# Optimization experiments

Measured on AMD Instinct MI355X. Metric: run time of the kernel, lower is better.

Reference implementation:

```python
import jax, jax.numpy as jnp
import numpy as np

NUM_USERS = 100000
NUM_ITEMS = 200000
IN_DIM = 128
HID = 256
E = 500000


def setup_inputs() -> dict:
    key = jax.random.key(0)
    ks = jax.random.split(key, 12)
    s1 = 1.0 / np.sqrt(2 * IN_DIM)
    s2 = 1.0 / np.sqrt(HID)
    return {
        "user_embed": jax.random.normal(ks[0], (NUM_USERS, IN_DIM), jnp.float32),
        "item_embed": jax.random.normal(ks[1], (NUM_ITEMS, IN_DIM), jnp.float32),
        "u_clicks": jax.random.randint(ks[2], (E,), 0, NUM_USERS, jnp.int32),
        "v_clicks": jax.random.randint(ks[3], (E,), 0, NUM_ITEMS, jnp.int32),
        "u_buys": jax.random.randint(ks[4], (E,), 0, NUM_USERS, jnp.int32),
        "v_buys": jax.random.randint(ks[5], (E,), 0, NUM_ITEMS, jnp.int32),
        "W1_clicks": jax.random.normal(ks[6], (2 * IN_DIM, HID), jnp.float32) * s1,
        "b1_clicks": jnp.zeros((HID,), jnp.float32),
        "W2_clicks": jax.random.normal(ks[7], (HID,), jnp.float32) * s2,
        "b2_clicks": jnp.zeros((1,), jnp.float32),
        "W1_buys": jax.random.normal(ks[8], (2 * IN_DIM, HID), jnp.float32) * s1,
        "b1_buys": jnp.zeros((HID,), jnp.float32),
        "W2_buys": jax.random.normal(ks[9], (HID,), jnp.float32) * s2,
        "b2_buys": jnp.zeros((1,), jnp.float32),
    }


def _edge_mlp(h_u, h_v, W1, b1, W2, b2):
    # concat([h_u, h_v]) @ W1 computed without materializing the concat:
    # split W1 into source-half and target-half. Dropout(p=0) is identity.
    d = h_u.shape[1]
    h = jax.nn.relu(h_u @ W1[:d] + h_v @ W1[d:] + b1)  # [E, HID]
    return h @ W2 + b2[0]  # [E] (Linear(hidden,1).squeeze(1))


def reference(user_embed, item_embed, u_clicks, v_clicks, u_buys, v_buys,
              W1_clicks, b1_clicks, W2_clicks, b2_clicks,
              W1_buys, b1_buys, W2_buys, b2_buys):
    logits_clicks = _edge_mlp(user_embed[u_clicks], item_embed[v_clicks],
                              W1_clicks, b1_clicks, W2_clicks, b2_clicks)
    logits_buys = _edge_mlp(user_embed[u_buys], item_embed[v_buys],
                            W1_buys, b1_buys, W2_buys, b2_buys)
    return logits_clicks, logits_buys
```

## Files before the change

kernel.cpp:

```cpp
#include <hip/hip_runtime.h>
#include <hip/hip_bf16.h>

typedef short bf16x8 __attribute__((ext_vector_type(8)));
typedef float f32x4 __attribute__((ext_vector_type(4)));
typedef unsigned int u32x4 __attribute__((ext_vector_type(4)));

#define HID 256
#define IN_DIM 128
#define M_BLOCK 64
#define NPERSIST 256

__device__ __forceinline__ float bf2f(unsigned short x) {
    union { unsigned int u; float f; } c; c.u = ((unsigned int)x) << 16; return c.f;
}
__device__ __forceinline__ unsigned short f2bf(float f) {
    union { float f; unsigned int u; } c; c.f = f;
    unsigned int u = c.u;
    u += 0x7FFFu + ((u >> 16) & 1u);
    return (unsigned short)(u >> 16);
}
__device__ __forceinline__ unsigned int pack2(float lo, float hi) {
    return (unsigned int)f2bf(lo) | ((unsigned int)f2bf(hi) << 16);
}

__device__ __forceinline__ void gload_lds16(const void* g, void* l) {
    __builtin_amdgcn_global_load_lds(
        (const __attribute__((address_space(1))) void*)g,
        (__attribute__((address_space(3))) void*)l,
        16, 0, 0);
}

__device__ __forceinline__ bool detect_bf16(const unsigned short* p, int strideElems) {
    const int lane = threadIdx.x & 63;
    unsigned int u = p[(size_t)2 * lane * strideElems];
    unsigned int e = (u >> 7) & 0xFFu;
    bool bad = ((u & 0x7FFFu) != 0u) && (e < 90u || e > 141u);
    return __ballot(bad) == 0ull;
}
__device__ __forceinline__ bool detect_idx64(const int* p) {
    const int lane = threadIdx.x & 63;
    int v = p[2 * (lane * 64) + 1];
    return __ballot(v != 0) == 0ull;
}

extern "C" __global__ void cvt_tables_kernel(
    const void* __restrict__ user_embed, const void* __restrict__ item_embed,
    unsigned short* __restrict__ uT, unsigned short* __restrict__ iT,
    long long nU8, long long nI8)
{
    const int t = blockIdx.y;
    const void* src = t ? item_embed : user_embed;
    unsigned short* dst = t ? iT : uT;
    const long long n8 = t ? nI8 : nU8;
    const bool bf = detect_bf16((const unsigned short*)src, 1024);
    long long i = (long long)blockIdx.x * 256 + threadIdx.x;
    const long long stride = (long long)gridDim.x * 256;
    if (bf) {
        const u32x4* s = (const u32x4*)src;
        for (; i < n8; i += stride)
            __builtin_nontemporal_store(s[i], reinterpret_cast<u32x4*>(dst + i * 8));
    } else {
        const float4* s = (const float4*)src;
        for (; i < n8; i += stride) {
            float4 f0 = s[2 * i];
            float4 f1 = s[2 * i + 1];
            u32x4 o;
            o.x = pack2(f0.x, f0.y);
            o.y = pack2(f0.z, f0.w);
            o.z = pack2(f1.x, f1.y);
            o.w = pack2(f1.z, f1.w);
            __builtin_nontemporal_store(o, reinterpret_cast<u32x4*>(dst + i * 8));
        }
    }
}

extern "C" __global__ void pack_w1_kernel(
    const void* __restrict__ W1c,
    const void* __restrict__ W1b,
    unsigned short* __restrict__ outp)
{
    const int t = blockIdx.y;
    const void* W1 = t ? W1b : W1c;
    const unsigned short* W1u = (const unsigned short*)W1;
    const float* W1f = (const float*)W1;
    const bool w1bf = detect_bf16(W1u, 512);

    const int tid = blockIdx.x * 256 + threadIdx.x;
    const int lane = tid & 63;
    const int nt = (tid >> 6) & 15;
    const int kt = tid >> 10;
    const int k0 = kt * 32 + (lane >> 4) * 8;
    const int n  = nt * 16 + (lane & 15);
    unsigned short vals[8];
#pragma unroll
    for (int j = 0; j < 8; ++j) {
        const int src = (k0 + j) * HID + n;
        vals[j] = w1bf ? W1u[src] : f2bf(W1f[src]);
    }
    unsigned short* dst = outp + (size_t)t * 65536 + (size_t)tid * 8;
    *reinterpret_cast<uint4*>(dst) = *reinterpret_cast<const uint4*>(vals);
}

extern "C" __global__ __launch_bounds__(256, 2)
void edge_mlp_kernel(
    const void* __restrict__ user_embed,
    const void* __restrict__ item_embed,
    const unsigned short* __restrict__ uT,
    const unsigned short* __restrict__ iT,
    const int* __restrict__ u0, const int* __restrict__ v0,
    const int* __restrict__ u1, const int* __restrict__ v1,
    const unsigned short* __restrict__ packedW1,
    const void* __restrict__ b1_0, const void* __restrict__ w2_0,
    const void* __restrict__ b2_0,
    const void* __restrict__ b1_1, const void* __restrict__ w2_1,
    const void* __restrict__ b2_1,
    float* __restrict__ out, int E, int useWs)
{
    __shared__ __attribute__((aligned(16))) unsigned short sA[2][32 * 64 * 8];
    __shared__ float pRed[4][M_BLOCK];

    const int t   = blockIdx.y;
    const int tid = threadIdx.x;
    const int lane = tid & 63;
    const int wv   = tid >> 6;
    const int lq = lane >> 4;
    const int lm = lane & 15;

    const int* uI = t ? u1 : u0;
    const int* vI = t ? v1 : v0;
    const void* b1 = t ? b1_1 : b1_0;
    const void* w2 = t ? w2_1 : w2_0;
    const void* b2 = t ? b2_1 : b2_0;
    const unsigned short* pW = packedW1 + (size_t)t * 65536;

    const bool w2Bf = detect_bf16((const unsigned short*)w2, 2);

    const int* gI = (wv < 2) ? uI : vI;
    const bool g64 = detect_idx64(gI);
    const int halfOff = (wv & 1) * 64;
    const unsigned short* tabW = (wv < 2) ? uT : iT;
    const void* tabRaw = (wv < 2) ? user_embed : item_embed;
    bool tbf = false;
    if (!useWs) tbf = detect_bf16((const unsigned short*)tabRaw, 1024);

    bf16x8 bFr[8][4];
#pragma unroll
    for (int kt = 0; kt < 8; ++kt)
#pragma unroll
        for (int ntg = 0; ntg < 4; ++ntg)
            bFr[kt][ntg] = *reinterpret_cast<const bf16x8*>(
                pW + (((size_t)(kt * 16 + wv * 4 + ntg) * 64 + lane) * 8));

    float b1v[4], w2v[4];
#pragma unroll
    for (int ntg = 0; ntg < 4; ++ntg) {
        const int n = (wv * 4 + ntg) * 16 + lm;
        b1v[ntg] = w2Bf ? bf2f(((const unsigned short*)b1)[n]) : ((const float*)b1)[n];
        w2v[ntg] = w2Bf ? bf2f(((const unsigned short*)w2)[n]) : ((const float*)w2)[n];
    }
    const float b2v = w2Bf ? bf2f(((const unsigned short*)b2)[0]) : ((const float*)b2)[0];

    const int ntiles = (E + M_BLOCK - 1) / M_BLOCK;

    auto gather_tile = [&](int tile, int buf) {
        const int e = tile * M_BLOCK + lane;
        const int eC = (e < E) ? e : (E - 1);
        const size_t idx = (size_t)(g64 ? gI[2 * eC] : gI[eC]);
        unsigned short* sbase = &sA[buf][(wv * 8) * 512];
        if (useWs) {
            const unsigned short* rowbase = tabW + idx * IN_DIM + halfOff;
#pragma unroll
            for (int c = 0; c < 8; ++c)
                gload_lds16(rowbase + c * 8, sbase + c * 512);
        } else if (tbf) {
            const unsigned short* rowbase =
                (const unsigned short*)tabRaw + idx * IN_DIM + halfOff;
#pragma unroll
            for (int c = 0; c < 8; ++c)
                gload_lds16(rowbase + c * 8, sbase + c * 512);
        } else {
            const float* rowbase = (const float*)tabRaw + idx * IN_DIM + halfOff;
#pragma unroll
            for (int c = 0; c < 8; ++c) {
                float4 f0 = *reinterpret_cast<const float4*>(rowbase + c * 8);
                float4 f1 = *reinterpret_cast<const float4*>(rowbase + c * 8 + 4);
                uint4 o;
                o.x = pack2(f0.x, f0.y);
                o.y = pack2(f0.z, f0.w);
                o.z = pack2(f1.x, f1.y);
                o.w = pack2(f1.z, f1.w);
                *reinterpret_cast<uint4*>(sbase + c * 512 + lane * 8) = o;
            }
        }
    };

    int ti = blockIdx.x;
    int cur = 0;
    if (ti < ntiles) gather_tile(ti, 0);
    __syncthreads();

    while (ti < ntiles) {
        const int tn = ti + gridDim.x;
        if (tn < ntiles) gather_tile(tn, cur ^ 1);

        f32x4 acc[4][4];
#pragma unroll
        for (int ms = 0; ms < 4; ++ms)
#pragma unroll
            for (int ntg = 0; ntg < 4; ++ntg)
                acc[ms][ntg] = (f32x4){0.f, 0.f, 0.f, 0.f};

        const unsigned short* sAc = sA[cur];
#pragma unroll
        for (int kt = 0; kt < 8; ++kt) {
            bf16x8 aF[4];
#pragma unroll
            for (int ms = 0; ms < 4; ++ms)
                aF[ms] = *reinterpret_cast<const bf16x8*>(
                    &sAc[(((kt * 4 + lq) * 64) + ms * 16 + lm) * 8]);
#pragma unroll
            for (int ntg = 0; ntg < 4; ++ntg)
#pragma unroll
                for (int ms = 0; ms < 4; ++ms)
                    acc[ms][ntg] = __builtin_amdgcn_mfma_f32_16x16x32_bf16(
                        aF[ms], bFr[kt][ntg], acc[ms][ntg], 0, 0, 0);
        }

        float part[4][4];
#pragma unroll
        for (int ms = 0; ms < 4; ++ms)
#pragma unroll
            for (int r = 0; r < 4; ++r) part[ms][r] = 0.f;

#pragma unroll
        for (int ntg = 0; ntg < 4; ++ntg)
#pragma unroll
            for (int ms = 0; ms < 4; ++ms)
#pragma unroll
                for (int r = 0; r < 4; ++r) {
                    float h = acc[ms][ntg][r] + b1v[ntg];
                    h = fmaxf(h, 0.f);
                    part[ms][r] = fmaf(h, w2v[ntg], part[ms][r]);
                }

#pragma unroll
        for (int off = 1; off < 16; off <<= 1) {
#pragma unroll
            for (int ms = 0; ms < 4; ++ms)
#pragma unroll
                for (int r = 0; r < 4; ++r)
                    part[ms][r] += __shfl_xor(part[ms][r], off, 64);
        }

        if (lm == 0) {
#pragma unroll
            for (int ms = 0; ms < 4; ++ms)
#pragma unroll
                for (int r = 0; r < 4; ++r)
                    pRed[wv][ms * 16 + lq * 4 + r] = part[ms][r];
        }
        __syncthreads();

        if (tid < M_BLOCK) {
            const int e = ti * M_BLOCK + tid;
            if (e < E) {
                float s = b2v + pRed[0][tid] + pRed[1][tid] + pRed[2][tid] + pRed[3][tid];
                out[(size_t)t * E + e] = s;
            }
        }
        __syncthreads();

        ti = tn;
        cur ^= 1;
    }
}

extern "C" void kernel_launch(void* const* d_in, const int* in_sizes, int n_in,
                              void* d_out, int out_size, void* d_ws, size_t ws_size,
                              hipStream_t stream)
{
    const void* user_embed = d_in[0];
    const void* item_embed = d_in[1];
    const int* u0 = (const int*)d_in[2];
    const int* v0 = (const int*)d_in[3];
    const int* u1 = (const int*)d_in[4];
    const int* v1 = (const int*)d_in[5];
    const void* W1c = d_in[6];
    const void* b1c = d_in[7];
    const void* w2c = d_in[8];
    const void* b2c = d_in[9];
    const void* W1b = d_in[10];
    const void* b1b = d_in[11];
    const void* w2b = d_in[12];
    const void* b2b = d_in[13];

    const int E = in_sizes[2];
    const size_t U = (size_t)in_sizes[0] / IN_DIM;
    const size_t I = (size_t)in_sizes[1] / IN_DIM;

    unsigned short* packedW1 = (unsigned short*)d_ws;
    unsigned short* uT = (unsigned short*)((char*)d_ws + 262144);
    unsigned short* iT = uT + U * IN_DIM;
    const size_t need = 262144 + (U + I) * IN_DIM * sizeof(unsigned short);
    const int useWs = (ws_size >= need) ? 1 : 0;

    if (useWs) {
        const long long nU8 = (long long)U * IN_DIM / 8;
        const long long nI8 = (long long)I * IN_DIM / 8;
        hipLaunchKernelGGL(cvt_tables_kernel, dim3(2048, 2), dim3(256), 0, stream,
                           user_embed, item_embed, uT, iT, nU8, nI8);
    }

    hipLaunchKernelGGL(pack_w1_kernel, dim3(32, 2), dim3(256), 0, stream, W1c, W1b, packedW1);

    hipLaunchKernelGGL(edge_mlp_kernel, dim3(NPERSIST, 2), dim3(256), 0, stream,
                       user_embed, item_embed, uT, iT, u0, v0, u1, v1, packedW1,
                       b1c, w2c, b2c, b1b, w2b, b2b,
                       (float*)d_out, E, useWs);
}
```

Before: 430.7 us.

## Coalesce row gathers via lane shuffles and XOR-swizzle LDS tile layout

The embedding gather now broadcasts edge indices with warp shuffles so groups of 8 lanes each fetch contiguous 16-byte chunks of the same row, instead of every lane striding through its own row. The LDS tile layout changes to a row-major, XOR-swizzled arrangement per wave section, and the MFMA A-fragment reads are re-indexed to match. The goal is better global-memory coalescing for the random row gathers while avoiding LDS bank conflicts. It adds shuffle and index arithmetic per load.

```diff
diff --git a/kernel.cpp b/kernel.cpp
--- a/kernel.cpp
+++ b/kernel.cpp
@@ -161,25 +161,25 @@
     const float b2v = w2Bf ? bf2f(((const unsigned short*)b2)[0]) : ((const float*)b2)[0];
 
     const int ntiles = (E + M_BLOCK - 1) / M_BLOCK;
+    const int grp  = lane >> 3;
+    const int subl = lane & 7;
+    const int csrc = subl ^ grp;
 
     auto gather_tile = [&](int tile, int buf) {
         const int e = tile * M_BLOCK + lane;
         const int eC = (e < E) ? e : (E - 1);
-        const size_t idx = (size_t)(g64 ? gI[2 * eC] : gI[eC]);
-        unsigned short* sbase = &sA[buf][(wv * 8) * 512];
-        if (useWs) {
-            const unsigned short* rowbase = tabW + idx * IN_DIM + halfOff;
-#pragma unroll
-            for (int c = 0; c < 8; ++c)
-                gload_lds16(rowbase + c * 8, sbase + c * 512);
-        } else if (tbf) {
-            const unsigned short* rowbase =
-                (const unsigned short*)tabRaw + idx * IN_DIM + halfOff;
-#pragma unroll
-            for (int c = 0; c < 8; ++c)
-                gload_lds16(rowbase + c * 8, sbase + c * 512);
+        const int myIdx = g64 ? gI[2 * eC] : gI[eC];
+        unsigned short* sbase = &sA[buf][wv * 4096];
+        if (useWs || tbf) {
+            const unsigned short* tab16 = useWs ? tabW : (const unsigned short*)tabRaw;
+            const int coff = halfOff + csrc * 8;
+#pragma unroll
+            for (int i = 0; i < 8; ++i) {
+                const int sIdx = __shfl(myIdx, i * 8 + grp, 64);
+                gload_lds16(tab16 + (size_t)sIdx * IN_DIM + coff, sbase + i * 512);
+            }
         } else {
-            const float* rowbase = (const float*)tabRaw + idx * IN_DIM + halfOff;
+            const float* rowbase = (const float*)tabRaw + (size_t)myIdx * IN_DIM + halfOff;
 #pragma unroll
             for (int c = 0; c < 8; ++c) {
                 float4 f0 = *reinterpret_cast<const float4*>(rowbase + c * 8);
@@ -189,7 +189,9 @@
                 o.y = pack2(f0.z, f0.w);
                 o.z = pack2(f1.x, f1.y);
                 o.w = pack2(f1.z, f1.w);
-                *reinterpret_cast<uint4*>(sbase + c * 512 + lane * 8) = o;
+                const int slot = c ^ subl;
+                *reinterpret_cast<uint4*>(
+                    sbase + grp * 512 + subl * 64 + slot * 8) = o;
             }
         }
     };
@@ -215,9 +217,15 @@
         for (int kt = 0; kt < 8; ++kt) {
             bf16x8 aF[4];
 #pragma unroll
-            for (int ms = 0; ms < 4; ++ms)
+            for (int ms = 0; ms < 4; ++ms) {
+                const int ch = kt * 32 + lq * 8;
+                const int wsec = ch >> 6;
+                const int c = (ch >> 3) & 7;
+                const int m = ms * 16 + lm;
+                const int slot = c ^ (m & 7);
                 aF[ms] = *reinterpret_cast<const bf16x8*>(
-                    &sAc[(((kt * 4 + lq) * 64) + ms * 16 + lm) * 8]);
+                    &sAc[wsec * 4096 + (m >> 3) * 512 + (m & 7) * 64 + slot * 8]);
+            }
 #pragma unroll
             for (int ntg = 0; ntg < 4; ++ntg)
 #pragma unroll
```

Result: slower. 457.2 us (+6.2%).

## Fuse table conversion, weight packing and edge MLP into one cooperative kernel

Applied to the files above, without the earlier changes.

Merges the three launches (embedding-table bf16 conversion, W1 packing, edge MLP) into a single cooperative kernel of 512 persistent blocks, using a grid-wide sync between the prep phase and the compute phase. The aim is to remove launch overhead and the gaps between kernels. The conversion stores also switch from nontemporal to normal stores, which may leave the converted tables in cache for the gather phase. In exchange, only 512 blocks do the table conversion, and the grid sync forces every block to wait for the slowest one. If the cooperative launch fails, the code falls back to the old three-kernel path.

```diff
diff --git a/kernel.cpp b/kernel.cpp
--- a/kernel.cpp
+++ b/kernel.cpp
@@ -1,5 +1,8 @@
 #include <hip/hip_runtime.h>
 #include <hip/hip_bf16.h>
+#include <hip/hip_cooperative_groups.h>
+
+namespace cg = cooperative_groups;
 
 typedef short bf16x8 __attribute__((ext_vector_type(8)));
 typedef float f32x4 __attribute__((ext_vector_type(4)));
@@ -43,25 +46,19 @@
     return __ballot(v != 0) == 0ull;
 }
 
-extern "C" __global__ void cvt_tables_kernel(
-    const void* __restrict__ user_embed, const void* __restrict__ item_embed,
-    unsigned short* __restrict__ uT, unsigned short* __restrict__ iT,
-    long long nU8, long long nI8)
-{
-    const int t = blockIdx.y;
-    const void* src = t ? item_embed : user_embed;
-    unsigned short* dst = t ? iT : uT;
-    const long long n8 = t ? nI8 : nU8;
+
+__device__ __forceinline__ void cvt_one_table(
+    const void* src, unsigned short* dst, long long n8,
+    long long g0, long long gs)
+{
     const bool bf = detect_bf16((const unsigned short*)src, 1024);
-    long long i = (long long)blockIdx.x * 256 + threadIdx.x;
-    const long long stride = (long long)gridDim.x * 256;
     if (bf) {
         const u32x4* s = (const u32x4*)src;
-        for (; i < n8; i += stride)
-            __builtin_nontemporal_store(s[i], reinterpret_cast<u32x4*>(dst + i * 8));
+        for (long long i = g0; i < n8; i += gs)
+            *reinterpret_cast<u32x4*>(dst + i * 8) = s[i];
     } else {
         const float4* s = (const float4*)src;
-        for (; i < n8; i += stride) {
+        for (long long i = g0; i < n8; i += gs) {
             float4 f0 = s[2 * i];
             float4 f1 = s[2 * i + 1];
             u32x4 o;
@@ -69,26 +66,20 @@
             o.y = pack2(f0.z, f0.w);
             o.z = pack2(f1.x, f1.y);
             o.w = pack2(f1.z, f1.w);
-            __builtin_nontemporal_store(o, reinterpret_cast<u32x4*>(dst + i * 8));
+            *reinterpret_cast<u32x4*>(dst + i * 8) = o;
         }
     }
 }
 
-extern "C" __global__ void pack_w1_kernel(
-    const void* __restrict__ W1c,
-    const void* __restrict__ W1b,
-    unsigned short* __restrict__ outp)
-{
-    const int t = blockIdx.y;
-    const void* W1 = t ? W1b : W1c;
+__device__ __forceinline__ void pack_w1_one(
+    const void* W1, unsigned short* outp, int tid13)
+{
     const unsigned short* W1u = (const unsigned short*)W1;
     const float* W1f = (const float*)W1;
     const bool w1bf = detect_bf16(W1u, 512);
-
-    const int tid = blockIdx.x * 256 + threadIdx.x;
-    const int lane = tid & 63;
-    const int nt = (tid >> 6) & 15;
-    const int kt = tid >> 10;
+    const int lane = tid13 & 63;
+    const int nt = (tid13 >> 6) & 15;
+    const int kt = tid13 >> 10;
     const int k0 = kt * 32 + (lane >> 4) * 8;
     const int n  = nt * 16 + (lane & 15);
     unsigned short vals[8];
@@ -97,16 +88,200 @@
         const int src = (k0 + j) * HID + n;
         vals[j] = w1bf ? W1u[src] : f2bf(W1f[src]);
     }
-    unsigned short* dst = outp + (size_t)t * 65536 + (size_t)tid * 8;
+    unsigned short* dst = outp + (size_t)tid13 * 8;
     *reinterpret_cast<uint4*>(dst) = *reinterpret_cast<const uint4*>(vals);
 }
+
+
+extern "C" __global__ void cvt_tables_kernel(
+    const void* __restrict__ user_embed, const void* __restrict__ item_embed,
+    unsigned short* __restrict__ uT, unsigned short* __restrict__ iT,
+    long long nU8, long long nI8)
+{
+    const int t = blockIdx.y;
+    const long long g0 = (long long)blockIdx.x * 256 + threadIdx.x;
+    const long long gs = (long long)gridDim.x * 256;
+    if (t == 0) cvt_one_table(user_embed, uT, nU8, g0, gs);
+    else        cvt_one_table(item_embed, iT, nI8, g0, gs);
+}
+
+extern "C" __global__ void pack_w1_kernel(
+    const void* __restrict__ W1c, const void* __restrict__ W1b,
+    unsigned short* __restrict__ outp)
+{
+    const int t = blockIdx.y;
+    const int tid13 = blockIdx.x * 256 + threadIdx.x;
+    pack_w1_one(t ? W1b : W1c, outp + (size_t)t * 65536, tid13);
+}
+
+
+struct EdgeCtx {
+    const void* user_embed; const void* item_embed;
+    const unsigned short* uT; const unsigned short* iT;
+    const int* uI; const int* vI;
+    const unsigned short* pW;
+    const void* b1; const void* w2; const void* b2;
+    float* out; int E; int useWs; int t;
+};
+
+template <int TILE_STRIDE_UNUSED = 0>
+__device__ __forceinline__ void edge_phase(
+    const EdgeCtx& c, int pb, int nPersist,
+    unsigned short (*sA)[32 * 64 * 8], float (*pRed)[M_BLOCK])
+{
+    const int tid = threadIdx.x;
+    const int lane = tid & 63;
+    const int wv   = tid >> 6;
+    const int lq = lane >> 4;
+    const int lm = lane & 15;
+
+    const bool w2Bf = detect_bf16((const unsigned short*)c.w2, 2);
+
+    const int* gI = (wv < 2) ? c.uI : c.vI;
+    const bool g64 = detect_idx64(gI);
+    const int halfOff = (wv & 1) * 64;
+    const unsigned short* tabW = (wv < 2) ? c.uT : c.iT;
+    const void* tabRaw = (wv < 2) ? c.user_embed : c.item_embed;
+    bool tbf = false;
+    if (!c.useWs) tbf = detect_bf16((const unsigned short*)tabRaw, 1024);
+
+    bf16x8 bFr[8][4];
+#pragma unroll
+    for (int kt = 0; kt < 8; ++kt)
+#pragma unroll
+        for (int ntg = 0; ntg < 4; ++ntg)
+            bFr[kt][ntg] = *reinterpret_cast<const bf16x8*>(
+                c.pW + (((size_t)(kt * 16 + wv * 4 + ntg) * 64 + lane) * 8));
+
+    float b1v[4], w2v[4];
+#pragma unroll
+    for (int ntg = 0; ntg < 4; ++ntg) {
+        const int n = (wv * 4 + ntg) * 16 + lm;
+        b1v[ntg] = w2Bf ? bf2f(((const unsigned short*)c.b1)[n]) : ((const float*)c.b1)[n];
+        w2v[ntg] = w2Bf ? bf2f(((const unsigned short*)c.w2)[n]) : ((const float*)c.w2)[n];
+    }
+    const float b2v = w2Bf ? bf2f(((const unsigned short*)c.b2)[0]) : ((const float*)c.b2)[0];
+
+    const int ntiles = (c.E + M_BLOCK - 1) / M_BLOCK;
+
+    auto gather_tile = [&](int tile, int buf) {
+        const int e = tile * M_BLOCK + lane;
+        const int eC = (e < c.E) ? e : (c.E - 1);
+        const size_t idx = (size_t)(g64 ? gI[2 * eC] : gI[eC]);
+        unsigned short* sbase = &sA[buf][(wv * 8) * 512];
+        if (c.useWs) {
+            const unsigned short* rowbase = tabW + idx * IN_DIM + halfOff;
+#pragma unroll
+            for (int ch = 0; ch < 8; ++ch)
+                gload_lds16(rowbase + ch * 8, sbase + ch * 512);
+        } else if (tbf) {
+            const unsigned short* rowbase =
+                (const unsigned short*)tabRaw + idx * IN_DIM + halfOff;
+#pragma unroll
+            for (int ch = 0; ch < 8; ++ch)
+                gload_lds16(rowbase + ch * 8, sbase + ch * 512);
+        } else {
+            const float* rowbase = (const float*)tabRaw + idx * IN_DIM + halfOff;
+#pragma unroll
+            for (int ch = 0; ch < 8; ++ch) {
+                float4 f0 = *reinterpret_cast<const float4*>(rowbase + ch * 8);
+                float4 f1 = *reinterpret_cast<const float4*>(rowbase + ch * 8 + 4);
+                uint4 o;
+                o.x = pack2(f0.x, f0.y);
+                o.y = pack2(f0.z, f0.w);
+                o.z = pack2(f1.x, f1.y);
+                o.w = pack2(f1.z, f1.w);
+                *reinterpret_cast<uint4*>(sbase + ch * 512 + lane * 8) = o;
+            }
+        }
+    };
+
+    int ti = pb;
+    int cur = 0;
+    if (ti < ntiles) gather_tile(ti, 0);
+    __syncthreads();
+
+    while (ti < ntiles) {
+        const int tn = ti + nPersist;
+        if (tn < ntiles) gather_tile(tn, cur ^ 1);
+
+        f32x4 acc[4][4];
+#pragma unroll
+        for (int ms = 0; ms < 4; ++ms)
+#pragma unroll
+            for (int ntg = 0; ntg < 4; ++ntg)
+                acc[ms][ntg] = (f32x4){0.f, 0.f, 0.f, 0.f};
+
+        const unsigned short* sAc = sA[cur];
+#pragma unroll
+        for (int kt = 0; kt < 8; ++kt) {
+            bf16x8 aF[4];
+#pragma unroll
+            for (int ms = 0; ms < 4; ++ms)
+                aF[ms] = *reinterpret_cast<const bf16x8*>(
+                    &sAc[(((kt * 4 + lq) * 64) + ms * 16 + lm) * 8]);
+#pragma unroll
+            for (int ntg = 0; ntg < 4; ++ntg)
+#pragma unroll
+                for (int ms = 0; ms < 4; ++ms)
+                    acc[ms][ntg] = __builtin_amdgcn_mfma_f32_16x16x32_bf16(
+                        aF[ms], bFr[kt][ntg], acc[ms][ntg], 0, 0, 0);
+        }
+
+        float part[4][4];
+#pragma unroll
+        for (int ms = 0; ms < 4; ++ms)
+#pragma unroll
+            for (int r = 0; r < 4; ++r) part[ms][r] = 0.f;
+
+#pragma unroll
+        for (int ntg = 0; ntg < 4; ++ntg)
+#pragma unroll
+            for (int ms = 0; ms < 4; ++ms)
+#pragma unroll
+                for (int r = 0; r < 4; ++r) {
+                    float h = acc[ms][ntg][r] + b1v[ntg];
+                    h = fmaxf(h, 0.f);
+                    part[ms][r] = fmaf(h, w2v[ntg], part[ms][r]);
+                }
+
+#pragma unroll
+        for (int off = 1; off < 16; off <<= 1) {
+#pragma unroll
+            for (int ms = 0; ms < 4; ++ms)
+#pragma unroll
+                for (int r = 0; r < 4; ++r)
+                    part[ms][r] += __shfl_xor(part[ms][r], off, 64);
+        }
+
+        if (lm == 0) {
+#pragma unroll
+            for (int ms = 0; ms < 4; ++ms)
+#pragma unroll
+                for (int r = 0; r < 4; ++r)
+                    pRed[wv][ms * 16 + lq * 4 + r] = part[ms][r];
+        }
+        __syncthreads();
+
+        if (tid < M_BLOCK) {
+            const int e = ti * M_BLOCK + tid;
+            if (e < c.E) {
+                float s = b2v + pRed[0][tid] + pRed[1][tid] + pRed[2][tid] + pRed[3][tid];
+                c.out[(size_t)c.t * c.E + e] = s;
+            }
+        }
+        __syncthreads();
+
+        ti = tn;
+        cur ^= 1;
+    }
+}
+
 
 extern "C" __global__ __launch_bounds__(256, 2)
 void edge_mlp_kernel(
-    const void* __restrict__ user_embed,
-    const void* __restrict__ item_embed,
-    const unsigned short* __restrict__ uT,
-    const unsigned short* __restrict__ iT,
+    const void* __restrict__ user_embed, const void* __restrict__ item_embed,
+    const unsigned short* __restrict__ uT, const unsigned short* __restrict__ iT,
     const int* __restrict__ u0, const int* __restrict__ v0,
     const int* __restrict__ u1, const int* __restrict__ v1,
     const unsigned short* __restrict__ packedW1,
@@ -118,161 +293,58 @@
 {
     __shared__ __attribute__((aligned(16))) unsigned short sA[2][32 * 64 * 8];
     __shared__ float pRed[4][M_BLOCK];
-
-    const int t   = blockIdx.y;
-    const int tid = threadIdx.x;
-    const int lane = tid & 63;
-    const int wv   = tid >> 6;
-    const int lq = lane >> 4;
-    const int lm = lane & 15;
-
-    const int* uI = t ? u1 : u0;
-    const int* vI = t ? v1 : v0;
-    const void* b1 = t ? b1_1 : b1_0;
-    const void* w2 = t ? w2_1 : w2_0;
-    const void* b2 = t ? b2_1 : b2_0;
-    const unsigned short* pW = packedW1 + (size_t)t * 65536;
-
-    const bool w2Bf = detect_bf16((const unsigned short*)w2, 2);
-
-    const int* gI = (wv < 2) ? uI : vI;
-    const bool g64 = detect_idx64(gI);
-    const int halfOff = (wv & 1) * 64;
-    const unsigned short* tabW = (wv < 2) ? uT : iT;
-    const void* tabRaw = (wv < 2) ? user_embed : item_embed;
-    bool tbf = false;
-    if (!useWs) tbf = detect_bf16((const unsigned short*)tabRaw, 1024);
-
-    bf16x8 bFr[8][4];
-#pragma unroll
-    for (int kt = 0; kt < 8; ++kt)
-#pragma unroll
-        for (int ntg = 0; ntg < 4; ++ntg)
-            bFr[kt][ntg] = *reinterpret_cast<const bf16x8*>(
-                pW + (((size_t)(kt * 16 + wv * 4 + ntg) * 64 + lane) * 8));
-
-    float b1v[4], w2v[4];
-#pragma unroll
-    for (int ntg = 0; ntg < 4; ++ntg) {
-        const int n = (wv * 4 + ntg) * 16 + lm;
-        b1v[ntg] = w2Bf ? bf2f(((const unsigned short*)b1)[n]) : ((const float*)b1)[n];
-        w2v[ntg] = w2Bf ? bf2f(((const unsigned short*)w2)[n]) : ((const float*)w2)[n];
+    const int t = blockIdx.y;
+    EdgeCtx c;
+    c.user_embed = user_embed; c.item_embed = item_embed;
+    c.uT = uT; c.iT = iT;
+    c.uI = t ? u1 : u0; c.vI = t ? v1 : v0;
+    c.pW = packedW1 + (size_t)t * 65536;
+    c.b1 = t ? b1_1 : b1_0; c.w2 = t ? w2_1 : w2_0; c.b2 = t ? b2_1 : b2_0;
+    c.out = out; c.E = E; c.useWs = useWs; c.t = t;
+    edge_phase(c, blockIdx.x, gridDim.x, sA, pRed);
+}
+
+
+extern "C" __global__ __launch_bounds__(256, 2)
+void fused_kernel(
+    const void* user_embed, const void* item_embed,
+    unsigned short* uT, unsigned short* iT,
+    const int* u0, const int* v0, const int* u1, const int* v1,
+    unsigned short* packedW1,
+    const void* W1c, const void* W1b,
+    const void* b1_0, const void* w2_0, const void* b2_0,
+    const void* b1_1, const void* w2_1, const void* b2_1,
+    float* out, int E, int useWs, long long nU8, long long nI8)
+{
+    __shared__ __attribute__((aligned(16))) unsigned short sA[2][32 * 64 * 8];
+    __shared__ float pRed[4][M_BLOCK];
+
+    {
+        const long long g0 = (long long)blockIdx.x * 256 + threadIdx.x;
+        const long long gs = (long long)gridDim.x * 256;
+        if (useWs) {
+            cvt_one_table(user_embed, uT, nU8, g0, gs);
+            cvt_one_table(item_embed, iT, nI8, g0, gs);
+        }
+        if (g0 < 16384) {
+            const int tt = (int)(g0 >> 13);
+            pack_w1_one(tt ? W1b : W1c, packedW1 + (size_t)tt * 65536, (int)(g0 & 8191));
+        }
     }
-    const float b2v = w2Bf ? bf2f(((const unsigned short*)b2)[0]) : ((const float*)b2)[0];
-
-    const int ntiles = (E + M_BLOCK - 1) / M_BLOCK;
-
-    auto gather_tile = [&](int tile, int buf) {
-        const int e = tile * M_BLOCK + lane;
-        const int eC = (e < E) ? e : (E - 1);
-        const size_t idx = (size_t)(g64 ? gI[2 * eC] : gI[eC]);
-        unsigned short* sbase = &sA[buf][(wv * 8) * 512];
-        if (useWs) {
-            const unsigned short* rowbase = tabW + idx * IN_DIM + halfOff;
-#pragma unroll
-            for (int c = 0; c < 8; ++c)
-                gload_lds16(rowbase + c * 8, sbase + c * 512);
-        } else if (tbf) {
-            const unsigned short* rowbase =
-                (const unsigned short*)tabRaw + idx * IN_DIM + halfOff;
-#pragma unroll
-            for (int c = 0; c < 8; ++c)
-                gload_lds16(rowbase + c * 8, sbase + c * 512);
-        } else {
-            const float* rowbase = (const float*)tabRaw + idx * IN_DIM + halfOff;
-#pragma unroll
-            for (int c = 0; c < 8; ++c) {
-                float4 f0 = *reinterpret_cast<const float4*>(rowbase + c * 8);
-                float4 f1 = *reinterpret_cast<const float4*>(rowbase + c * 8 + 4);
-                uint4 o;
-                o.x = pack2(f0.x, f0.y);
-                o.y = pack2(f0.z, f0.w);
-                o.z = pack2(f1.x, f1.y);
-                o.w = pack2(f1.z, f1.w);
-                *reinterpret_cast<uint4*>(sbase + c * 512 + lane * 8) = o;
-            }
-        }
-    };
-
-    int ti = blockIdx.x;
-    int cur = 0;
-    if (ti < ntiles) gather_tile(ti, 0);
-    __syncthreads();
-
-    while (ti < ntiles) {
-        const int tn = ti + gridDim.x;
-        if (tn < ntiles) gather_tile(tn, cur ^ 1);
-
-        f32x4 acc[4][4];
-#pragma unroll
-        for (int ms = 0; ms < 4; ++ms)
-#pragma unroll
-            for (int ntg = 0; ntg < 4; ++ntg)
-                acc[ms][ntg] = (f32x4){0.f, 0.f, 0.f, 0.f};
-
-        const unsigned short* sAc = sA[cur];
-#pragma unroll
-        for (int kt = 0; kt < 8; ++kt) {
-            bf16x8 aF[4];
-#pragma unroll
-            for (int ms = 0; ms < 4; ++ms)
-                aF[ms] = *reinterpret_cast<const bf16x8*>(
-                    &sAc[(((kt * 4 + lq) * 64) + ms * 16 + lm) * 8]);
-#pragma unroll
-            for (int ntg = 0; ntg < 4; ++ntg)
-#pragma unroll
-                for (int ms = 0; ms < 4; ++ms)
-                    acc[ms][ntg] = __builtin_amdgcn_mfma_f32_16x16x32_bf16(
-                        aF[ms], bFr[kt][ntg], acc[ms][ntg], 0, 0, 0);
-        }
-
-        float part[4][4];
-#pragma unroll
-        for (int ms = 0; ms < 4; ++ms)
-#pragma unroll
-            for (int r = 0; r < 4; ++r) part[ms][r] = 0.f;
-
-#pragma unroll
-        for (int ntg = 0; ntg < 4; ++ntg)
-#pragma unroll
-            for (int ms = 0; ms < 4; ++ms)
-#pragma unroll
-                for (int r = 0; r < 4; ++r) {
-                    float h = acc[ms][ntg][r] + b1v[ntg];
-                    h = fmaxf(h, 0.f);
-                    part[ms][r] = fmaf(h, w2v[ntg], part[ms][r]);
-                }
-
-#pragma unroll
-        for (int off = 1; off < 16; off <<= 1) {
-#pragma unroll
-            for (int ms = 0; ms < 4; ++ms)
-#pragma unroll
-                for (int r = 0; r < 4; ++r)
-                    part[ms][r] += __shfl_xor(part[ms][r], off, 64);
-        }
-
-        if (lm == 0) {
-#pragma unroll
-            for (int ms = 0; ms < 4; ++ms)
-#pragma unroll
-                for (int r = 0; r < 4; ++r)
-                    pRed[wv][ms * 16 + lq * 4 + r] = part[ms][r];
-        }
-        __syncthreads();
-
-        if (tid < M_BLOCK) {
-            const int e = ti * M_BLOCK + tid;
-            if (e < E) {
-                float s = b2v + pRed[0][tid] + pRed[1][tid] + pRed[2][tid] + pRed[3][tid];
-                out[(size_t)t * E + e] = s;
-            }
-        }
-        __syncthreads();
-
-        ti = tn;
-        cur ^= 1;
-    }
+    __threadfence();
+    cg::this_grid().sync();
+
+    const int b = blockIdx.x;
+    const int t = b >> 8;
+    const int pb = b & 255;
+    EdgeCtx c;
+    c.user_embed = user_embed; c.item_embed = item_embed;
+    c.uT = uT; c.iT = iT;
+    c.uI = t ? u1 : u0; c.vI = t ? v1 : v0;
+    c.pW = packedW1 + (size_t)t * 65536;
+    c.b1 = t ? b1_1 : b1_0; c.w2 = t ? w2_1 : w2_0; c.b2 = t ? b2_1 : b2_0;
+    c.out = out; c.E = E; c.useWs = useWs; c.t = t;
+    edge_phase(c, pb, NPERSIST, sA, pRed);
 }
 
 extern "C" void kernel_launch(void* const* d_in, const int* in_sizes, int n_in,
@@ -302,19 +374,29 @@
     unsigned short* uT = (unsigned short*)((char*)d_ws + 262144);
     unsigned short* iT = uT + U * IN_DIM;
     const size_t need = 262144 + (U + I) * IN_DIM * sizeof(unsigned short);
-    const int useWs = (ws_size >= need) ? 1 : 0;
-
-    if (useWs) {
-        const long long nU8 = (long long)U * IN_DIM / 8;
-        const long long nI8 = (long long)I * IN_DIM / 8;
+    int useWs = (ws_size >= need) ? 1 : 0;
+    long long nU8 = (long long)U * IN_DIM / 8;
+    long long nI8 = (long long)I * IN_DIM / 8;
+    float* outp = (float*)d_out;
+
+    void* kargs[] = {
+        (void*)&user_embed, (void*)&item_embed, (void*)&uT, (void*)&iT,
+        (void*)&u0, (void*)&v0, (void*)&u1, (void*)&v1,
+        (void*)&packedW1, (void*)&W1c, (void*)&W1b,
+        (void*)&b1c, (void*)&w2c, (void*)&b2c,
+        (void*)&b1b, (void*)&w2b, (void*)&b2b,
+        (void*)&outp, (void*)&E, (void*)&useWs, (void*)&nU8, (void*)&nI8
+    };
+    hipError_t err = hipLaunchCooperativeKernel(
+        reinterpret_cast<const void*>(fused_kernel),
+        dim3(2 * NPERSIST), dim3(256), kargs, 0, stream);
+    if (err == hipSuccess) return;
+
+    if (useWs)
         hipLaunchKernelGGL(cvt_tables_kernel, dim3(2048, 2), dim3(256), 0, stream,
                            user_embed, item_embed, uT, iT, nU8, nI8);
-    }
-
     hipLaunchKernelGGL(pack_w1_kernel, dim3(32, 2), dim3(256), 0, stream, W1c, W1b, packedW1);
-
     hipLaunchKernelGGL(edge_mlp_kernel, dim3(NPERSIST, 2), dim3(256), 0, stream,
                        user_embed, item_embed, uT, iT, u0, v0, u1, v1, packedW1,
-                       b1c, w2c, b2c, b1b, w2b, b2b,
-                       (float*)d_out, E, useWs);
-}
+                       b1c, w2c, b2c, b1b, w2b, b2b, outp, E, useWs);
+}
```

New measurement: 563.1 us. +30.7%, slower.
